# Optimization experiments

Hardware: AMD Instinct MI355X
Metric: run time of the kernel (lower is better)

The kernel has to match this reference:

```python
import jax, jax.numpy as jnp
import numpy as np

B, C, H, W = 8, 512, 48, 48
DK = C // 8            # query/key dim
L = max(H, W)          # rel_pos_length == H == W
R = 2 * L - 1          # num relative shifts
N = H * W
EPS = 1e-5


def setup_inputs() -> dict:
    key = jax.random.key(0)
    ks = jax.random.split(key, 20)
    d = {
        "x": jax.random.normal(ks[0], (B, C, H, W), jnp.float32),
        "Wq": jax.random.normal(ks[1], (DK, C), jnp.float32) * 0.02,
        "bq": jnp.zeros((DK,), jnp.float32),
        "q_scale": jnp.ones((DK,), jnp.float32),
        "q_bias": jnp.zeros((DK,), jnp.float32),
        "Wk": jax.random.normal(ks[2], (DK, C), jnp.float32) * 0.02,
        "bk": jnp.zeros((DK,), jnp.float32),
        "k_scale": jnp.ones((DK,), jnp.float32),
        "k_bias": jnp.zeros((DK,), jnp.float32),
        "Wv": jax.random.normal(ks[3], (C, C), jnp.float32) * 0.02,
        "bv": jnp.zeros((C,), jnp.float32),
        "v_scale": jnp.ones((C,), jnp.float32),
        "v_bias": jnp.zeros((C,), jnp.float32),
        "rel_rows": jax.random.normal(ks[4], (R, DK), jnp.float32),
        "rel_columns": jax.random.normal(ks[5], (R, DK), jnp.float32),
        "bnr_scale": jnp.ones((C,), jnp.float32),
        "bnr_bias": jnp.zeros((C,), jnp.float32),
        "bnc_scale": jnp.ones((C,), jnp.float32),
        "bnc_bias": jnp.zeros((C,), jnp.float32),
        # gamma is a learned scalar (init 0 in torch; nonzero here so output != x)
        "gamma": jax.random.normal(ks[6], (1,), jnp.float32) * 0.1,
    }
    return d


def _bn(y, scale, bias):
    # train-mode BatchNorm2d: batch stats over (B,H,W), biased variance
    m = jnp.mean(y, axis=(0, 2, 3))
    v = jnp.mean((y - m[None, :, None, None]) ** 2, axis=(0, 2, 3))
    yn = (y - m[None, :, None, None]) * jax.lax.rsqrt(v + EPS)[None, :, None, None]
    return yn * scale[None, :, None, None] + bias[None, :, None, None]


def _conv_bn_relu(x, Wc, bc, scale, bias):
    y = jnp.einsum('bchw,oc->bohw', x, Wc) + bc[None, :, None, None]  # 1x1 conv
    return jax.nn.relu(_bn(y, scale, bias))


def _rel_P(l, rel_table):
    # compute_reindexing_tensor reduces to a one-hot over shift (i - x) since
    # |i-x| <= L always holds when L == l; Ih @ rel_table == gather by shift.
    x = jnp.arange(l)[:, None]
    i = jnp.arange(l)[None, :]
    idx = i - x + (L - 1)                 # (l, l) in [0, 2L-2]
    return rel_table[idx]                 # (l, l, DK)


def reference(x, Wq, bq, q_scale, q_bias, Wk, bk, k_scale, k_bias,
              Wv, bv, v_scale, v_bias, rel_rows, rel_columns,
              bnr_scale, bnr_bias, bnc_scale, bnc_bias, gamma):
    q = _conv_bn_relu(x, Wq, bq, q_scale, q_bias).reshape(B, DK, N)   # proj_query^T
    k = _conv_bn_relu(x, Wk, bk, k_scale, k_bias).reshape(B, DK, N)
    v = _conv_bn_relu(x, Wv, bv, v_scale, v_bias).reshape(B, C, N)

    energy = jnp.einsum('bdn,bdm->bnm', q, k)        # (B,N,N) = Q^T K (unscaled)
    attention = jax.nn.softmax(energy, axis=-1)
    out = jnp.einsum('bcj,bij->bci', v, attention)   # V A^T
    attn_mask = out.reshape(B, C, H, W)

    # relative position terms: Eh = V (Ph Q^T), Ew = V (Pw Q^T)
    Ph = _rel_P(H, rel_rows).reshape(N, DK)          # (N,DK) since H==W
    Mh = jnp.einsum('nd,bdm->bnm', Ph, q)
    Eh = jnp.einsum('bcn,bnm->bcm', v, Mh).reshape(B, C, H, W)
    Eh = _bn(Eh, bnr_scale, bnr_bias)

    Pw = _rel_P(W, rel_columns).reshape(N, DK)
    Mw = jnp.einsum('nd,bdm->bnm', Pw, q)
    Ew = jnp.einsum('bcn,bnm->bcm', v, Mw).reshape(B, C, H, W)
    Ew = _bn(Ew, bnc_scale, bnc_bias)

    attn_mask = attn_mask + Eh + Ew
    return gamma[0] * attn_mask + x
```

## Files before the change

### kernel.cpp

```cpp
#include <hip/hip_runtime.h>
#include <math.h>

#define BB   8
#define CIN  512
#define NSP  2304
#define OCH  640
#define LL   48

typedef __attribute__((ext_vector_type(8))) short bf16x8;
typedef __attribute__((ext_vector_type(8))) unsigned short u16x8;
typedef __attribute__((ext_vector_type(4))) float f32x4;

__device__ inline unsigned short f2bf(float f) {
  unsigned int u = __float_as_uint(f);
  unsigned int r = (u + 0x7fffu + ((u >> 16) & 1u)) >> 16;
  return (unsigned short)r;
}
__device__ inline float bf2f(unsigned short h) {
  return __uint_as_float(((unsigned int)h) << 16);
}


#define STAGE128x64(GP, LD, LDSN)                                              \
  {                                                                            \
    const unsigned short* gsrc_ = (GP);                                        \
    _Pragma("unroll") for (int cc_ = 0; cc_ < 4; cc_++) {                      \
      int base_ = w * 2048 + cc_ * 512;                                        \
      int row_ = w * 32 + cc_ * 8 + rsub;                                      \
      __builtin_amdgcn_global_load_lds(                                        \
          (const __attribute__((address_space(1))) void*)(gsrc_ +              \
              (size_t)row_ * (LD) + scolb),                                    \
          (__attribute__((address_space(3))) void*)&(LDSN)[base_], 16, 0, 0);  \
    }                                                                          \
  }

#define STAGE8(GPA, LDA, LA, GPB, LDB, LB)                                     \
  {                                                                            \
    if (w < 4) {                                                               \
      const unsigned short* gsrc_ = (GPA);                                     \
      _Pragma("unroll") for (int cc_ = 0; cc_ < 4; cc_++) {                    \
        int base_ = w * 2048 + cc_ * 512;                                      \
        int row_ = w * 32 + cc_ * 8 + rsub;                                    \
        __builtin_amdgcn_global_load_lds(                                      \
            (const __attribute__((address_space(1))) void*)(gsrc_ +            \
                (size_t)row_ * (LDA) + scolb),                                 \
            (__attribute__((address_space(3))) void*)&(LA)[base_], 16, 0, 0);  \
      }                                                                        \
    } else {                                                                   \
      const unsigned short* gsrc_ = (GPB);                                     \
      int w2_ = w - 4;                                                         \
      _Pragma("unroll") for (int cc_ = 0; cc_ < 4; cc_++) {                    \
        int base_ = w2_ * 2048 + cc_ * 512;                                    \
        int row_ = w2_ * 32 + cc_ * 8 + rsub;                                  \
        __builtin_amdgcn_global_load_lds(                                      \
            (const __attribute__((address_space(1))) void*)(gsrc_ +            \
                (size_t)row_ * (LDB) + scolb),                                 \
            (__attribute__((address_space(3))) void*)&(LB)[base_], 16, 0, 0);  \
      }                                                                        \
    }                                                                          \
  }

#define MFMA_STEP(APTR, BPTR)                                                  \
  _Pragma("unroll") for (int kk_ = 0; kk_ < 2; kk_++) {                        \
    bf16x8 af_[4], bf_[4];                                                     \
    int kcol_ = (((kk_ * 4 + (lane >> 4)) ^ (lane & 7)) * 8);                  \
    _Pragma("unroll") for (int m_ = 0; m_ < 4; m_++)                           \
      af_[m_] = *(const bf16x8*)&(APTR)[(wr * 64 + m_ * 16 + (lane & 15)) * 64 + kcol_]; \
    _Pragma("unroll") for (int n_ = 0; n_ < 4; n_++)                           \
      bf_[n_] = *(const bf16x8*)&(BPTR)[(wc * 64 + n_ * 16 + (lane & 15)) * 64 + kcol_]; \
    _Pragma("unroll") for (int m_ = 0; m_ < 4; m_++)                           \
      _Pragma("unroll") for (int n_ = 0; n_ < 4; n_++)                         \
        acc[m_][n_] = __builtin_amdgcn_mfma_f32_16x16x32_bf16(                 \
            af_[m_], bf_[n_], acc[m_][n_], 0, 0, 0);                           \
  }

#define MFMA_STEP8(APTR, BPTR)                                                 \
  _Pragma("unroll") for (int kk_ = 0; kk_ < 2; kk_++) {                        \
    bf16x8 af_[4], bf_[2];                                                     \
    int kcol_ = (((kk_ * 4 + (lane >> 4)) ^ (lane & 7)) * 8);                  \
    _Pragma("unroll") for (int m_ = 0; m_ < 4; m_++)                           \
      af_[m_] = *(const bf16x8*)&(APTR)[(wr * 64 + m_ * 16 + (lane & 15)) * 64 + kcol_]; \
    _Pragma("unroll") for (int n_ = 0; n_ < 2; n_++)                           \
      bf_[n_] = *(const bf16x8*)&(BPTR)[(wc * 32 + n_ * 16 + (lane & 15)) * 64 + kcol_]; \
    _Pragma("unroll") for (int m_ = 0; m_ < 4; m_++)                           \
      _Pragma("unroll") for (int n_ = 0; n_ < 2; n_++)                         \
        acc[m_][n_] = __builtin_amdgcn_mfma_f32_16x16x32_bf16(                 \
            af_[m_], bf_[n_], acc[m_][n_], 0, 0, 0);                           \
  }

#define MFMA_PROLOG()                                                          \
  const int tid = threadIdx.x;                                                 \
  const int lane = tid & 63;                                                   \
  const int w = tid >> 6;                                                      \
  const int wr = w >> 1, wc = w & 1;                                           \
  const int rsub = lane >> 3;                                                  \
  const int scolb = ((lane & 7) ^ rsub) * 8;                                   \
  f32x4 acc[4][4] = {};                                                        \
  (void)scolb; (void)rsub; (void)wr; (void)wc;

__global__ __launch_bounds__(256) void prep_all(
    const float* __restrict__ Wq, const float* __restrict__ bq,
    const float* __restrict__ Wk, const float* __restrict__ bk,
    const float* __restrict__ Wv, const float* __restrict__ bv,
    const float* __restrict__ rel_rows, const float* __restrict__ rel_cols,
    unsigned short* __restrict__ Wstb, float* __restrict__ bst,
    unsigned short* __restrict__ Pcatb) {
  int idx = blockIdx.x * 256 + threadIdx.x;
  if (idx < OCH * CIN) {
    int row = idx >> 9;
    float val;
    if (row < 64)       val = Wq[idx];
    else if (row < 128) val = Wk[idx - (64 << 9)];
    else                val = Wv[idx - (128 << 9)];
    Wstb[idx] = f2bf(val);
    if (idx < OCH) {
      float bval;
      if (idx < 64)       bval = bq[idx];
      else if (idx < 128) bval = bk[idx - 64];
      else                bval = bv[idx - 128];
      bst[idx] = bval;
    }
  } else {
    int p = idx - OCH * CIN;
    int dd = p / NSP;
    int n = p - dd * NSP;
    int xr = n / LL;
    int ic = n - xr * LL;
    int shift = ic - xr + (LL - 1);
    float val = (dd < 64) ? rel_rows[shift * 64 + dd]
                          : rel_cols[shift * 64 + (dd - 64)];
    Pcatb[p] = f2bf(val);
  }
}

__global__ __launch_bounds__(256) void transpose_x(
    const float* __restrict__ x, unsigned short* __restrict__ xTb) {
  __shared__ float t[64][65];
  const int n0 = blockIdx.x * 64;
  const int c0 = blockIdx.y * 64;
  const int b = blockIdx.z;
  const int j = threadIdx.x & 63;
  const int g = threadIdx.x >> 6;
  const float* xp = x + (size_t)b * CIN * NSP;
#pragma unroll
  for (int i = 0; i < 16; i++) {
    int cl = g * 16 + i;
    t[cl][j] = xp[(size_t)(c0 + cl) * NSP + n0 + j];
  }
  __syncthreads();
  unsigned short* op = xTb + (size_t)b * NSP * CIN;
#pragma unroll
  for (int i = 0; i < 16; i++) {
    int nl = g * 16 + i;
    op[(size_t)(n0 + nl) * CIN + c0 + j] = f2bf(t[j][nl]);
  }
}

__global__ __launch_bounds__(256) void proj_mfma(
    const unsigned short* __restrict__ Wstb, const float* __restrict__ bst,
    const unsigned short* __restrict__ xTb, unsigned short* __restrict__ y16,
    float* __restrict__ part1, float* __restrict__ part2) {
  __shared__ unsigned short As[2][8192];
  __shared__ unsigned short Bs[2][8192];
  int sw = ((blockIdx.x & 7) * 90) + (blockIdx.x >> 3);
  const int rb = sw % 5;
  const int nb = (sw / 5) % 18;
  const int b = sw / 90;
  const int r0 = rb * 128;
  const int n0 = nb * 128;
  MFMA_PROLOG();
  const unsigned short* A = Wstb + (size_t)r0 * CIN;
  const unsigned short* B = xTb + (size_t)b * NSP * CIN + (size_t)n0 * CIN;

  STAGE128x64(A, CIN, As[0]);
  STAGE128x64(B, CIN, Bs[0]);
  STAGE128x64(A + 64, CIN, As[1]);
  STAGE128x64(B + 64, CIN, Bs[1]);
  asm volatile("s_waitcnt vmcnt(8)" ::: "memory");
  __builtin_amdgcn_sched_barrier(0);
  __builtin_amdgcn_s_barrier();

  int cur = 0;
  for (int t = 0; t < 8; ++t) {
    __builtin_amdgcn_s_setprio(1);
    MFMA_STEP(As[cur], Bs[cur]);
    __builtin_amdgcn_s_setprio(0);
    __builtin_amdgcn_sched_barrier(0);
    __builtin_amdgcn_s_barrier();
    if (t + 2 < 8) {
      STAGE128x64(A + (t + 2) * 64, CIN, As[cur]);
      STAGE128x64(B + (t + 2) * 64, CIN, Bs[cur]);
      asm volatile("s_waitcnt vmcnt(8)" ::: "memory");
    } else {
      asm volatile("s_waitcnt vmcnt(0)" ::: "memory");
    }
    __builtin_amdgcn_sched_barrier(0);
    __builtin_amdgcn_s_barrier();
    cur ^= 1;
  }

  float* sp = (float*)&As[0][0];
#pragma unroll
  for (int m = 0; m < 4; m++) {
#pragma unroll
    for (int r = 0; r < 4; r++) {
      int rl = wr * 64 + m * 16 + (lane >> 4) * 4 + r;
      int row = r0 + rl;
      float bias = bst[row];
      float s1 = 0.f, s2 = 0.f;
#pragma unroll
      for (int n = 0; n < 4; n++) {
        float yv = acc[m][n][r] + bias;
        s1 += yv;
        s2 += yv * yv;
        y16[((size_t)b * OCH + row) * NSP + n0 + wc * 64 + n * 16 + (lane & 15)] = f2bf(yv);
      }
#pragma unroll
      for (int off = 1; off < 16; off <<= 1) {
        s1 += __shfl_xor(s1, off);
        s2 += __shfl_xor(s2, off);
      }
      if ((lane & 15) == 0) {
        sp[rl * 2 + wc] = s1;
        sp[256 + rl * 2 + wc] = s2;
      }
    }
  }
  __syncthreads();
  if (tid < 128) {
    size_t pbase = ((size_t)b * 18 + nb) * OCH + r0 + tid;
    part1[pbase] = sp[tid * 2] + sp[tid * 2 + 1];
    part2[pbase] = sp[256 + tid * 2] + sp[256 + tid * 2 + 1];
  }
}

__global__ __launch_bounds__(256) void bn_finalize(
    const float* __restrict__ part1, const float* __restrict__ part2,
    const float* __restrict__ qs_, const float* __restrict__ qb_,
    const float* __restrict__ ks_, const float* __restrict__ kb_,
    const float* __restrict__ vs_, const float* __restrict__ vb_,
    float* __restrict__ chanA, float* __restrict__ chanB) {
  const int ch = blockIdx.x;
  const int tid = threadIdx.x;
  float s1 = 0.f, s2 = 0.f;
  for (int t = tid; t < 144; t += 256) {
    s1 += part1[(size_t)t * OCH + ch];
    s2 += part2[(size_t)t * OCH + ch];
  }
  __shared__ float sb[8];
#pragma unroll
  for (int off = 32; off > 0; off >>= 1) {
    s1 += __shfl_down(s1, off);
    s2 += __shfl_down(s2, off);
  }
  int lane = tid & 63, wid = tid >> 6;
  if (lane == 0) { sb[wid] = s1; sb[4 + wid] = s2; }
  __syncthreads();
  if (tid == 0) {
    float ts  = sb[0] + sb[1] + sb[2] + sb[3];
    float ts2 = sb[4] + sb[5] + sb[6] + sb[7];
    const float inv = 1.f / (float)(BB * NSP);
    float mean = ts * inv;
    float var  = ts2 * inv - mean * mean;
    float scale, bias;
    if (ch < 64)       { scale = qs_[ch];       bias = qb_[ch]; }
    else if (ch < 128) { scale = ks_[ch - 64];  bias = kb_[ch - 64]; }
    else               { scale = vs_[ch - 128]; bias = vb_[ch - 128]; }
    float a = scale * rsqrtf(var + 1e-5f);
    chanA[ch] = a;
    chanB[ch] = bias - mean * a;
  }
}

__global__ __launch_bounds__(256) void bnrelu_all(
    unsigned short* __restrict__ y16, const float* __restrict__ chanA,
    const float* __restrict__ chanB) {
  size_t i = ((size_t)blockIdx.x * 256 + threadIdx.x) * 8;
  int ch = (int)((i / NSP) % OCH);
  float a = chanA[ch], bo = chanB[ch];
  ushort4 u0 = *(ushort4*)&y16[i];
  ushort4 u1 = *(ushort4*)&y16[i + 4];
  ushort4 o0, o1;
  o0.x = f2bf(fmaxf(0.f, a * bf2f(u0.x) + bo));
  o0.y = f2bf(fmaxf(0.f, a * bf2f(u0.y) + bo));
  o0.z = f2bf(fmaxf(0.f, a * bf2f(u0.z) + bo));
  o0.w = f2bf(fmaxf(0.f, a * bf2f(u0.w) + bo));
  o1.x = f2bf(fmaxf(0.f, a * bf2f(u1.x) + bo));
  o1.y = f2bf(fmaxf(0.f, a * bf2f(u1.y) + bo));
  o1.z = f2bf(fmaxf(0.f, a * bf2f(u1.z) + bo));
  o1.w = f2bf(fmaxf(0.f, a * bf2f(u1.w) + bo));
  *(ushort4*)&y16[i] = o0;
  *(ushort4*)&y16[i + 4] = o1;
}

__global__ __launch_bounds__(256) void tr_qk(
    const unsigned short* __restrict__ y16, unsigned short* __restrict__ qTb,
    unsigned short* __restrict__ kTb) {
  __shared__ unsigned short t[64][72];
  const int n0 = blockIdx.x * 64;
  const int qk = blockIdx.y;
  const int b = blockIdx.z;
  const int j = threadIdx.x & 63;
  const int g = threadIdx.x >> 6;
#pragma unroll
  for (int i = 0; i < 16; i++) {
    int cl = g * 16 + i;
    t[cl][j] = y16[((size_t)b * OCH + qk * 64 + cl) * NSP + n0 + j];
  }
  __syncthreads();
  unsigned short* out = (qk == 0) ? qTb : kTb;
#pragma unroll
  for (int i = 0; i < 16; i++) {
    int nl = g * 16 + i;
    out[((size_t)b * NSP + n0 + nl) * 64 + j] = t[j][nl];
  }
}

__global__ __launch_bounds__(256) void qsum_kernel(
    const unsigned short* __restrict__ y16, float* __restrict__ qs) {
  int bd = blockIdx.x;
  int b = bd >> 6, d = bd & 63;
  const ushort4* p = (const ushort4*)(y16 + ((size_t)b * OCH + d) * NSP);
  float s = 0.f;
  for (int t = threadIdx.x; t < NSP / 4; t += 256) {
    ushort4 u = p[t];
    s += bf2f(u.x) + bf2f(u.y) + bf2f(u.z) + bf2f(u.w);
  }
  __shared__ float sb[4];
#pragma unroll
  for (int off = 32; off > 0; off >>= 1) s += __shfl_down(s, off);
  int lane = threadIdx.x & 63, wid = threadIdx.x >> 6;
  if (lane == 0) sb[wid] = s;
  __syncthreads();
  if (threadIdx.x == 0) qs[bd] = sb[0] + sb[1] + sb[2] + sb[3];
}

__global__ __launch_bounds__(256) void gq_mfma(
    const unsigned short* __restrict__ y16, float* __restrict__ Gqp) {
  __shared__ float wlds[4 * 4096];
  const int bx = blockIdx.x;
  const int b = bx >> 2, kc = bx & 3;
  const int tid = threadIdx.x;
  const int lane = tid & 63;
  const int w = tid >> 6;
  const unsigned short* q = y16 + (size_t)b * OCH * NSP;
  f32x4 acc[4][4] = {};
  for (int k0 = kc * 576 + w * 32; k0 < (kc + 1) * 576; k0 += 128) {
    bf16x8 fr[4];
#pragma unroll
    for (int f = 0; f < 4; f++) {
      int row = f * 16 + (lane & 15);
      fr[f] = *(const bf16x8*)&q[(size_t)row * NSP + k0 + (lane >> 4) * 8];
    }
#pragma unroll
    for (int fm = 0; fm < 4; fm++)
#pragma unroll
      for (int fn = 0; fn < 4; fn++)
        acc[fm][fn] = __builtin_amdgcn_mfma_f32_16x16x32_bf16(
            fr[fm], fr[fn], acc[fm][fn], 0, 0, 0);
  }
#pragma unroll
  for (int fm = 0; fm < 4; fm++)
#pragma unroll
    for (int fn = 0; fn < 4; fn++)
#pragma unroll
      for (int r = 0; r < 4; r++) {
        int d = fm * 16 + (lane >> 4) * 4 + r;
        int e = fn * 16 + (lane & 15);
        wlds[w * 4096 + d * 64 + e] = acc[fm][fn][r];
      }
  __syncthreads();
  for (int t = tid; t < 4096; t += 256)
    Gqp[(size_t)bx * 4096 + t] =
        wlds[t] + wlds[4096 + t] + wlds[8192 + t] + wlds[12288 + t];
}

__global__ __launch_bounds__(256) void energy_mfma(
    const unsigned short* __restrict__ qTb, const unsigned short* __restrict__ kTb,
    unsigned short* __restrict__ Pp, float* __restrict__ Ppart) {
  __shared__ unsigned short As[8192];
  __shared__ unsigned short Bs[8192];
  int sw = ((blockIdx.x & 7) * 324) + (blockIdx.x >> 3);
  const int jb = sw % 18;
  const int ib = (sw / 18) % 18;
  const int b = sw / 324;
  const int i0 = ib * 128;
  const int j0 = jb * 128;
  MFMA_PROLOG();
  STAGE128x64(qTb + ((size_t)b * NSP + i0) * 64, 64, As);
  STAGE128x64(kTb + ((size_t)b * NSP + j0) * 64, 64, Bs);
  __syncthreads();
  MFMA_STEP(As, Bs);
  __syncthreads();
  float* sp = (float*)As;
  unsigned short* pp = Pp + (size_t)b * NSP * NSP;
#pragma unroll
  for (int m = 0; m < 4; m++) {
#pragma unroll
    for (int r = 0; r < 4; r++) {
      int rl = wr * 64 + m * 16 + (lane >> 4) * 4 + r;
      int i = i0 + rl;
      float s1 = 0.f;
#pragma unroll
      for (int n = 0; n < 4; n++) {
        int j = j0 + wc * 64 + n * 16 + (lane & 15);
        unsigned short h = f2bf(__expf(acc[m][n][r]));
        pp[(size_t)i * NSP + j] = h;
        s1 += bf2f(h);
      }
#pragma unroll
      for (int off = 1; off < 16; off <<= 1) s1 += __shfl_xor(s1, off);
      if ((lane & 15) == 0) sp[rl * 2 + wc] = s1;
    }
  }
  __syncthreads();
  if (tid < 128)
    Ppart[((size_t)b * 18 + jb) * NSP + i0 + tid] = sp[tid * 2] + sp[tid * 2 + 1];
}

__global__ __launch_bounds__(256) void zred_kernel(
    const float* __restrict__ Ppart, float* __restrict__ rZ) {
  int row = blockIdx.x * 256 + threadIdx.x;
  int b = row / NSP, i = row % NSP;
  float s = 0.f;
#pragma unroll
  for (int jb = 0; jb < 18; jb++) s += Ppart[((size_t)b * 18 + jb) * NSP + i];
  rZ[row] = 1.f / s;
}

__global__ __launch_bounds__(256) void up_mfma(
    const unsigned short* __restrict__ y16, const unsigned short* __restrict__ Pcatb,
    float* __restrict__ Upart) {
  __shared__ unsigned short As[2][8192];
  __shared__ unsigned short Bs[2][8192];
  int sw = ((blockIdx.x & 7) * 24) + (blockIdx.x >> 3);
  const int cb = sw % 4;
  const int kc = (sw / 4) % 6;
  const int b = sw / 24;
  const int c0 = cb * 128;
  MFMA_PROLOG();
  const unsigned short* A = y16 + ((size_t)b * OCH + 128 + c0) * NSP + kc * 384;
  const unsigned short* B = Pcatb + kc * 384;

  STAGE128x64(A, NSP, As[0]);
  STAGE128x64(B, NSP, Bs[0]);
  STAGE128x64(A + 64, NSP, As[1]);
  STAGE128x64(B + 64, NSP, Bs[1]);
  asm volatile("s_waitcnt vmcnt(8)" ::: "memory");
  __builtin_amdgcn_sched_barrier(0);
  __builtin_amdgcn_s_barrier();

  int cur = 0;
  for (int t = 0; t < 6; ++t) {
    __builtin_amdgcn_s_setprio(1);
    MFMA_STEP(As[cur], Bs[cur]);
    __builtin_amdgcn_s_setprio(0);
    __builtin_amdgcn_sched_barrier(0);
    __builtin_amdgcn_s_barrier();
    if (t + 2 < 6) {
      STAGE128x64(A + (t + 2) * 64, NSP, As[cur]);
      STAGE128x64(B + (t + 2) * 64, NSP, Bs[cur]);
      asm volatile("s_waitcnt vmcnt(8)" ::: "memory");
    } else {
      asm volatile("s_waitcnt vmcnt(0)" ::: "memory");
    }
    __builtin_amdgcn_sched_barrier(0);
    __builtin_amdgcn_s_barrier();
    cur ^= 1;
  }

  float* up = Upart + ((size_t)kc * BB + b) * CIN * 128 + (size_t)c0 * 128;
#pragma unroll
  for (int m = 0; m < 4; m++)
#pragma unroll
    for (int r = 0; r < 4; r++) {
      int rl = wr * 64 + m * 16 + (lane >> 4) * 4 + r;
#pragma unroll
      for (int n = 0; n < 4; n++) {
        int col = wc * 64 + n * 16 + (lane & 15);
        up[(size_t)rl * 128 + col] = acc[m][n][r];
      }
    }
}

__global__ __launch_bounds__(256) void rel_finalize(
    const float* __restrict__ Upart, const float* __restrict__ Gqp,
    const float* __restrict__ qs,
    const float* __restrict__ bnr_s, const float* __restrict__ bnr_b,
    const float* __restrict__ bnc_s, const float* __restrict__ bnc_b,
    float* __restrict__ offc, unsigned short* __restrict__ Ucb) {
  const int c = blockIdx.x;
  const int tid = threadIdx.x;
  __shared__ float U[8][128];
  __shared__ float ghw[2];
  for (int t = tid; t < 1024; t += 256) {
    int b = t >> 7, dd = t & 127;
    float s = 0.f;
#pragma unroll
    for (int kc = 0; kc < 6; kc++)
      s += Upart[(((size_t)kc * BB + b) * CIN + c) * 128 + dd];
    U[b][dd] = s;
  }
  __syncthreads();
  if (tid < 64) {
    const int d = tid;
    float s1h = 0.f, s2h = 0.f, s1w = 0.f, s2w = 0.f;
    for (int b = 0; b < BB; b++) {
      float uh = U[b][d], uw = U[b][64 + d];
      float th = 0.f, tw = 0.f;
#pragma unroll
      for (int kc = 0; kc < 4; kc++) {
        const float* G = Gqp + ((size_t)(b * 4 + kc)) * 4096 + d * 64;
        for (int e = 0; e < 64; e++) {
          float g = G[e];
          th += g * U[b][e];
          tw += g * U[b][64 + e];
        }
      }
      float qsd = qs[b * 64 + d];
      s1h += uh * qsd;
      s2h += uh * th;
      s1w += uw * qsd;
      s2w += uw * tw;
    }
#pragma unroll
    for (int off = 32; off > 0; off >>= 1) {
      s1h += __shfl_down(s1h, off);
      s2h += __shfl_down(s2h, off);
      s1w += __shfl_down(s1w, off);
      s2w += __shfl_down(s2w, off);
    }
    if (d == 0) {
      const float inv = 1.f / (float)(BB * NSP);
      float mh = s1h * inv, vh = s2h * inv - mh * mh;
      float mw = s1w * inv, vw = s2w * inv - mw * mw;
      float gch = bnr_s[c] * rsqrtf(vh + 1e-5f);
      float gcw = bnc_s[c] * rsqrtf(vw + 1e-5f);
      ghw[0] = gch;
      ghw[1] = gcw;
      offc[c] = (bnr_b[c] - mh * gch) + (bnc_b[c] - mw * gcw);
    }
  }
  __syncthreads();
  for (int t = tid; t < 512; t += 256) {
    int b = t >> 6, d = t & 63;
    Ucb[((size_t)b * CIN + c) * 64 + d] =
        f2bf(U[b][d] * ghw[0] + U[b][64 + d] * ghw[1]);
  }
}

__global__ __launch_bounds__(512) void attn_fused_gemm(
    const unsigned short* __restrict__ y16,
    const unsigned short* __restrict__ Pp,
    const float* __restrict__ rZ,
    const unsigned short* __restrict__ Ucb,
    const unsigned short* __restrict__ qTb,
    const float* __restrict__ offc,
    const float* __restrict__ gammap,
    const float* __restrict__ x,
    float* __restrict__ dst) {
  __shared__ unsigned short As[2][8192];
  __shared__ unsigned short Bs[2][8192];
  int sw = ((blockIdx.x & 7) * 72) + (blockIdx.x >> 3);
  const int cb = sw % 4;
  const int ib = (sw / 4) % 18;
  const int b = sw / 72;
  const int c0 = cb * 128;
  const int i0 = ib * 128;
  const int tid = threadIdx.x;
  const int lane = tid & 63;
  const int w = tid >> 6;
  const int wr = w >> 2, wc = w & 3;
  const int rsub = lane >> 3;
  const int scolb = ((lane & 7) ^ rsub) * 8;
  f32x4 acc[4][2] = {};

  const unsigned short* A = y16 + ((size_t)b * OCH + 128 + c0) * NSP;
  const unsigned short* B = Pp + (size_t)b * NSP * NSP + (size_t)i0 * NSP;
  const unsigned short* A2 = Ucb + (size_t)b * CIN * 64 + (size_t)c0 * 64;
  const unsigned short* B2 = qTb + (size_t)b * NSP * 64 + (size_t)i0 * 64;

  STAGE8(A, NSP, As[0], B, NSP, Bs[0]);
  STAGE8(A + 64, NSP, As[1], B + 64, NSP, Bs[1]);
  asm volatile("s_waitcnt vmcnt(4)" ::: "memory");
  __builtin_amdgcn_sched_barrier(0);
  __builtin_amdgcn_s_barrier();

  int cur = 0;
  for (int tt = 0; tt < 37; ++tt) {
    if (tt == 36) {
#pragma unroll
      for (int n = 0; n < 2; n++) {
        float rz = rZ[(size_t)b * NSP + i0 + wc * 32 + n * 16 + (lane & 15)];
#pragma unroll
        for (int m = 0; m < 4; m++)
#pragma unroll
          for (int r = 0; r < 4; r++) acc[m][n][r] *= rz;
      }
    }
    __builtin_amdgcn_s_setprio(1);
    MFMA_STEP8(As[cur], Bs[cur]);
    __builtin_amdgcn_s_setprio(0);
    __builtin_amdgcn_sched_barrier(0);
    __builtin_amdgcn_s_barrier();
    if (tt + 2 < 36) {
      STAGE8(A + (tt + 2) * 64, NSP, As[cur], B + (tt + 2) * 64, NSP, Bs[cur]);
      asm volatile("s_waitcnt vmcnt(4)" ::: "memory");
    } else if (tt + 2 == 36) {
      STAGE8(A2, 64, As[cur], B2, 64, Bs[cur]);
      asm volatile("s_waitcnt vmcnt(4)" ::: "memory");
    } else {
      asm volatile("s_waitcnt vmcnt(0)" ::: "memory");
    }
    __builtin_amdgcn_sched_barrier(0);
    __builtin_amdgcn_s_barrier();
    cur ^= 1;
  }

  const float gmm = gammap[0];
  const float* xp = x + (size_t)b * CIN * NSP;
  float* dp = dst + (size_t)b * CIN * NSP;
#pragma unroll
  for (int m = 0; m < 4; m++) {
#pragma unroll
    for (int r = 0; r < 4; r++) {
      int c = c0 + wr * 64 + m * 16 + (lane >> 4) * 4 + r;
      float off = offc[c];
#pragma unroll
      for (int n = 0; n < 2; n++) {
        int i = i0 + wc * 32 + n * 16 + (lane & 15);
        size_t o = (size_t)c * NSP + i;
        dp[o] = gmm * (acc[m][n][r] + off) + xp[o];
      }
    }
  }
}

extern "C" void kernel_launch(void* const* d_in, const int* in_sizes, int n_in,
                              void* d_out, int out_size, void* d_ws, size_t ws_size,
                              hipStream_t stream) {
  const float* x        = (const float*)d_in[0];
  const float* Wq       = (const float*)d_in[1];
  const float* bq       = (const float*)d_in[2];
  const float* q_scale  = (const float*)d_in[3];
  const float* q_bias   = (const float*)d_in[4];
  const float* Wk       = (const float*)d_in[5];
  const float* bk       = (const float*)d_in[6];
  const float* k_scale  = (const float*)d_in[7];
  const float* k_bias   = (const float*)d_in[8];
  const float* Wv       = (const float*)d_in[9];
  const float* bv       = (const float*)d_in[10];
  const float* v_scale  = (const float*)d_in[11];
  const float* v_bias   = (const float*)d_in[12];
  const float* rel_rows = (const float*)d_in[13];
  const float* rel_cols = (const float*)d_in[14];
  const float* bnr_s    = (const float*)d_in[15];
  const float* bnr_b    = (const float*)d_in[16];
  const float* bnc_s    = (const float*)d_in[17];
  const float* bnc_b    = (const float*)d_in[18];
  const float* gamma    = (const float*)d_in[19];
  float* dst = (float*)d_out;

  float* ws = (float*)d_ws;
  size_t o = 0;
  unsigned short* Wstb = (unsigned short*)(ws + o); o += (size_t)OCH * CIN / 2;
  float* bst    = ws + o; o += 1024;
  float* chanA  = ws + o; o += 1024;
  float* chanB  = ws + o; o += 1024;
  unsigned short* Pcatb = (unsigned short*)(ws + o); o += (size_t)128 * NSP / 2;
  unsigned short* y16 = (unsigned short*)(ws + o); o += (size_t)BB * OCH * NSP / 2;
  unsigned short* xTb = (unsigned short*)(ws + o); o += (size_t)BB * NSP * CIN / 2;
  unsigned short* Pp  = (unsigned short*)(ws + o); o += (size_t)BB * NSP * NSP / 2;
  float* Ppart  = ws + o; o += (size_t)BB * 18 * NSP;
  float* rZ     = ws + o; o += (size_t)BB * NSP;
  float* Upart  = ws + o; o += (size_t)6 * BB * CIN * 128;
  float* Gqp    = ws + o; o += (size_t)32 * 4096;
  float* part1  = ws + o; o += (size_t)BB * 18 * OCH;
  float* part2  = ws + o; o += (size_t)BB * 18 * OCH;
  float* qs     = ws + o; o += 1024;
  float* offc   = ws + o; o += 1024;
  unsigned short* qTb = (unsigned short*)(ws + o); o += (size_t)BB * NSP * 64 / 2;
  unsigned short* kTb = (unsigned short*)(ws + o); o += (size_t)BB * NSP * 64 / 2;
  unsigned short* Ucb = (unsigned short*)(ws + o); o += (size_t)BB * CIN * 64 / 2;

  prep_all<<<(OCH * CIN + 128 * NSP) / 256, 256, 0, stream>>>(
      Wq, bq, Wk, bk, Wv, bv, rel_rows, rel_cols, Wstb, bst, Pcatb);
  transpose_x<<<dim3(NSP / 64, CIN / 64, BB), 256, 0, stream>>>(x, xTb);

  proj_mfma<<<720, 256, 0, stream>>>(Wstb, bst, xTb, y16, part1, part2);
  bn_finalize<<<OCH, 256, 0, stream>>>(part1, part2, q_scale, q_bias, k_scale,
                                       k_bias, v_scale, v_bias, chanA, chanB);
  bnrelu_all<<<(int)((size_t)BB * OCH * NSP / 8 / 256), 256, 0, stream>>>(y16, chanA, chanB);
  tr_qk<<<dim3(NSP / 64, 2, BB), 256, 0, stream>>>(y16, qTb, kTb);
  qsum_kernel<<<BB * 64, 256, 0, stream>>>(y16, qs);
  gq_mfma<<<32, 256, 0, stream>>>(y16, Gqp);

  energy_mfma<<<2592, 256, 0, stream>>>(qTb, kTb, Pp, Ppart);
  zred_kernel<<<BB * NSP / 256, 256, 0, stream>>>(Ppart, rZ);

  up_mfma<<<192, 256, 0, stream>>>(y16, Pcatb, Upart);
  rel_finalize<<<CIN, 256, 0, stream>>>(Upart, Gqp, qs, bnr_s, bnr_b,
                                        bnc_s, bnc_b, offc, Ucb);

  attn_fused_gemm<<<576, 512, 0, stream>>>(y16, Pp, rZ, Ucb, qTb, offc, gamma, x, dst);
}
```

Measured before the change: 237.9 us.

## Fuse BN-ReLU with Q/K transpose, fold Z reduction into final GEMM, restructure prefetch

Merges the BN+ReLU pass and the Q/K transpose into one kernel that keeps the Q/K tile in shared memory, which removes a full re-read of y16 for the transpose. The softmax normalizer reduction moves into the prologue of the final attention GEMM, so the separate zred kernel and the rZ buffer go away. The GEMM loops also change from a two-stage-ahead prefetch issued after the barrier to a one-stage-ahead prefetch issued before the MFMAs, with a full vmcnt(0) wait each step. That pipeline change may expose more load latency, and each of the 576 final blocks now recomputes its 128 reciprocals.

```diff
diff --git a/kernel.cpp b/kernel.cpp
--- a/kernel.cpp
+++ b/kernel.cpp
@@ -174,26 +174,20 @@
 
   STAGE128x64(A, CIN, As[0]);
   STAGE128x64(B, CIN, Bs[0]);
-  STAGE128x64(A + 64, CIN, As[1]);
-  STAGE128x64(B + 64, CIN, Bs[1]);
-  asm volatile("s_waitcnt vmcnt(8)" ::: "memory");
+  asm volatile("s_waitcnt vmcnt(0)" ::: "memory");
   __builtin_amdgcn_sched_barrier(0);
   __builtin_amdgcn_s_barrier();
 
   int cur = 0;
   for (int t = 0; t < 8; ++t) {
+    if (t + 1 < 8) {
+      STAGE128x64(A + (t + 1) * 64, CIN, As[cur ^ 1]);
+      STAGE128x64(B + (t + 1) * 64, CIN, Bs[cur ^ 1]);
+    }
     __builtin_amdgcn_s_setprio(1);
     MFMA_STEP(As[cur], Bs[cur]);
     __builtin_amdgcn_s_setprio(0);
-    __builtin_amdgcn_sched_barrier(0);
-    __builtin_amdgcn_s_barrier();
-    if (t + 2 < 8) {
-      STAGE128x64(A + (t + 2) * 64, CIN, As[cur]);
-      STAGE128x64(B + (t + 2) * 64, CIN, Bs[cur]);
-      asm volatile("s_waitcnt vmcnt(8)" ::: "memory");
-    } else {
-      asm volatile("s_waitcnt vmcnt(0)" ::: "memory");
-    }
+    asm volatile("s_waitcnt vmcnt(0)" ::: "memory");
     __builtin_amdgcn_sched_barrier(0);
     __builtin_amdgcn_s_barrier();
     cur ^= 1;
@@ -272,47 +266,51 @@
   }
 }
 
-__global__ __launch_bounds__(256) void bnrelu_all(
+__global__ __launch_bounds__(256) void bn_post(
     unsigned short* __restrict__ y16, const float* __restrict__ chanA,
-    const float* __restrict__ chanB) {
-  size_t i = ((size_t)blockIdx.x * 256 + threadIdx.x) * 8;
-  int ch = (int)((i / NSP) % OCH);
-  float a = chanA[ch], bo = chanB[ch];
-  ushort4 u0 = *(ushort4*)&y16[i];
-  ushort4 u1 = *(ushort4*)&y16[i + 4];
-  ushort4 o0, o1;
-  o0.x = f2bf(fmaxf(0.f, a * bf2f(u0.x) + bo));
-  o0.y = f2bf(fmaxf(0.f, a * bf2f(u0.y) + bo));
-  o0.z = f2bf(fmaxf(0.f, a * bf2f(u0.z) + bo));
-  o0.w = f2bf(fmaxf(0.f, a * bf2f(u0.w) + bo));
-  o1.x = f2bf(fmaxf(0.f, a * bf2f(u1.x) + bo));
-  o1.y = f2bf(fmaxf(0.f, a * bf2f(u1.y) + bo));
-  o1.z = f2bf(fmaxf(0.f, a * bf2f(u1.z) + bo));
-  o1.w = f2bf(fmaxf(0.f, a * bf2f(u1.w) + bo));
-  *(ushort4*)&y16[i] = o0;
-  *(ushort4*)&y16[i + 4] = o1;
-}
-
-__global__ __launch_bounds__(256) void tr_qk(
-    const unsigned short* __restrict__ y16, unsigned short* __restrict__ qTb,
+    const float* __restrict__ chanB, unsigned short* __restrict__ qTb,
     unsigned short* __restrict__ kTb) {
-  __shared__ unsigned short t[64][72];
+  __shared__ unsigned short qk[128][64];
   const int n0 = blockIdx.x * 64;
-  const int qk = blockIdx.y;
-  const int b = blockIdx.z;
-  const int j = threadIdx.x & 63;
-  const int g = threadIdx.x >> 6;
-#pragma unroll
-  for (int i = 0; i < 16; i++) {
-    int cl = g * 16 + i;
-    t[cl][j] = y16[((size_t)b * OCH + qk * 64 + cl) * NSP + n0 + j];
-  }
-  __syncthreads();
-  unsigned short* out = (qk == 0) ? qTb : kTb;
-#pragma unroll
-  for (int i = 0; i < 16; i++) {
-    int nl = g * 16 + i;
-    out[((size_t)b * NSP + n0 + nl) * 64 + j] = t[j][nl];
+  const int b = blockIdx.y;
+  const int tid = threadIdx.x;
+#pragma unroll
+  for (int k = 0; k < 20; k++) {
+    int v = tid + k * 256;
+    int ch = v >> 3;
+    int n8 = (v & 7) * 8;
+    size_t off = ((size_t)b * OCH + ch) * NSP + n0 + n8;
+    float a = chanA[ch], bo = chanB[ch];
+    ushort4 u0 = *(ushort4*)&y16[off];
+    ushort4 u1 = *(ushort4*)&y16[off + 4];
+    ushort4 o0, o1;
+    o0.x = f2bf(fmaxf(0.f, a * bf2f(u0.x) + bo));
+    o0.y = f2bf(fmaxf(0.f, a * bf2f(u0.y) + bo));
+    o0.z = f2bf(fmaxf(0.f, a * bf2f(u0.z) + bo));
+    o0.w = f2bf(fmaxf(0.f, a * bf2f(u0.w) + bo));
+    o1.x = f2bf(fmaxf(0.f, a * bf2f(u1.x) + bo));
+    o1.y = f2bf(fmaxf(0.f, a * bf2f(u1.y) + bo));
+    o1.z = f2bf(fmaxf(0.f, a * bf2f(u1.z) + bo));
+    o1.w = f2bf(fmaxf(0.f, a * bf2f(u1.w) + bo));
+    *(ushort4*)&y16[off] = o0;
+    *(ushort4*)&y16[off + 4] = o1;
+    if (ch < 128) {
+      *(ushort4*)&qk[ch][n8] = o0;
+      *(ushort4*)&qk[ch][n8 + 4] = o1;
+    }
+  }
+  __syncthreads();
+#pragma unroll
+  for (int it = 0; it < 4; it++) {
+    int combo = (tid >> 6) + it * 4;
+    int plane = combo >> 3;
+    int dg = combo & 7;
+    int nl = tid & 63;
+    unsigned short tmp[8];
+#pragma unroll
+    for (int d = 0; d < 8; d++) tmp[d] = qk[plane * 64 + dg * 8 + d][nl];
+    unsigned short* out = (plane == 0) ? qTb : kTb;
+    *(u16x8*)&out[((size_t)b * NSP + n0 + nl) * 64 + dg * 8] = *(u16x8*)tmp;
   }
 }
 
@@ -418,16 +416,6 @@
     Ppart[((size_t)b * 18 + jb) * NSP + i0 + tid] = sp[tid * 2] + sp[tid * 2 + 1];
 }
 
-__global__ __launch_bounds__(256) void zred_kernel(
-    const float* __restrict__ Ppart, float* __restrict__ rZ) {
-  int row = blockIdx.x * 256 + threadIdx.x;
-  int b = row / NSP, i = row % NSP;
-  float s = 0.f;
-#pragma unroll
-  for (int jb = 0; jb < 18; jb++) s += Ppart[((size_t)b * 18 + jb) * NSP + i];
-  rZ[row] = 1.f / s;
-}
-
 __global__ __launch_bounds__(256) void up_mfma(
     const unsigned short* __restrict__ y16, const unsigned short* __restrict__ Pcatb,
     float* __restrict__ Upart) {
@@ -444,26 +432,20 @@
 
   STAGE128x64(A, NSP, As[0]);
   STAGE128x64(B, NSP, Bs[0]);
-  STAGE128x64(A + 64, NSP, As[1]);
-  STAGE128x64(B + 64, NSP, Bs[1]);
-  asm volatile("s_waitcnt vmcnt(8)" ::: "memory");
+  asm volatile("s_waitcnt vmcnt(0)" ::: "memory");
   __builtin_amdgcn_sched_barrier(0);
   __builtin_amdgcn_s_barrier();
 
   int cur = 0;
   for (int t = 0; t < 6; ++t) {
+    if (t + 1 < 6) {
+      STAGE128x64(A + (t + 1) * 64, NSP, As[cur ^ 1]);
+      STAGE128x64(B + (t + 1) * 64, NSP, Bs[cur ^ 1]);
+    }
     __builtin_amdgcn_s_setprio(1);
     MFMA_STEP(As[cur], Bs[cur]);
     __builtin_amdgcn_s_setprio(0);
-    __builtin_amdgcn_sched_barrier(0);
-    __builtin_amdgcn_s_barrier();
-    if (t + 2 < 6) {
-      STAGE128x64(A + (t + 2) * 64, NSP, As[cur]);
-      STAGE128x64(B + (t + 2) * 64, NSP, Bs[cur]);
-      asm volatile("s_waitcnt vmcnt(8)" ::: "memory");
-    } else {
-      asm volatile("s_waitcnt vmcnt(0)" ::: "memory");
-    }
+    asm volatile("s_waitcnt vmcnt(0)" ::: "memory");
     __builtin_amdgcn_sched_barrier(0);
     __builtin_amdgcn_s_barrier();
     cur ^= 1;
@@ -552,7 +534,7 @@
 __global__ __launch_bounds__(512) void attn_fused_gemm(
     const unsigned short* __restrict__ y16,
     const unsigned short* __restrict__ Pp,
-    const float* __restrict__ rZ,
+    const float* __restrict__ Ppart,
     const unsigned short* __restrict__ Ucb,
     const unsigned short* __restrict__ qTb,
     const float* __restrict__ offc,
@@ -561,6 +543,7 @@
     float* __restrict__ dst) {
   __shared__ unsigned short As[2][8192];
   __shared__ unsigned short Bs[2][8192];
+  __shared__ float rzl[128];
   int sw = ((blockIdx.x & 7) * 72) + (blockIdx.x >> 3);
   const int cb = sw % 4;
   const int ib = (sw / 4) % 18;
@@ -581,17 +564,28 @@
   const unsigned short* B2 = qTb + (size_t)b * NSP * 64 + (size_t)i0 * 64;
 
   STAGE8(A, NSP, As[0], B, NSP, Bs[0]);
-  STAGE8(A + 64, NSP, As[1], B + 64, NSP, Bs[1]);
-  asm volatile("s_waitcnt vmcnt(4)" ::: "memory");
+  if (tid < 128) {
+    float s = 0.f;
+#pragma unroll
+    for (int jb = 0; jb < 18; jb++)
+      s += Ppart[((size_t)b * 18 + jb) * NSP + i0 + tid];
+    rzl[tid] = 1.f / s;
+  }
+  asm volatile("s_waitcnt vmcnt(0)" ::: "memory");
   __builtin_amdgcn_sched_barrier(0);
   __builtin_amdgcn_s_barrier();
 
   int cur = 0;
   for (int tt = 0; tt < 37; ++tt) {
+    if (tt + 1 < 36) {
+      STAGE8(A + (tt + 1) * 64, NSP, As[cur ^ 1], B + (tt + 1) * 64, NSP, Bs[cur ^ 1]);
+    } else if (tt + 1 == 36) {
+      STAGE8(A2, 64, As[cur ^ 1], B2, 64, Bs[cur ^ 1]);
+    }
     if (tt == 36) {
 #pragma unroll
       for (int n = 0; n < 2; n++) {
-        float rz = rZ[(size_t)b * NSP + i0 + wc * 32 + n * 16 + (lane & 15)];
+        float rz = rzl[wc * 32 + n * 16 + (lane & 15)];
 #pragma unroll
         for (int m = 0; m < 4; m++)
 #pragma unroll
@@ -601,17 +595,7 @@
     __builtin_amdgcn_s_setprio(1);
     MFMA_STEP8(As[cur], Bs[cur]);
     __builtin_amdgcn_s_setprio(0);
-    __builtin_amdgcn_sched_barrier(0);
-    __builtin_amdgcn_s_barrier();
-    if (tt + 2 < 36) {
-      STAGE8(A + (tt + 2) * 64, NSP, As[cur], B + (tt + 2) * 64, NSP, Bs[cur]);
-      asm volatile("s_waitcnt vmcnt(4)" ::: "memory");
-    } else if (tt + 2 == 36) {
-      STAGE8(A2, 64, As[cur], B2, 64, Bs[cur]);
-      asm volatile("s_waitcnt vmcnt(4)" ::: "memory");
-    } else {
-      asm volatile("s_waitcnt vmcnt(0)" ::: "memory");
-    }
+    asm volatile("s_waitcnt vmcnt(0)" ::: "memory");
     __builtin_amdgcn_sched_barrier(0);
     __builtin_amdgcn_s_barrier();
     cur ^= 1;
@@ -672,7 +656,6 @@
   unsigned short* xTb = (unsigned short*)(ws + o); o += (size_t)BB * NSP * CIN / 2;
   unsigned short* Pp  = (unsigned short*)(ws + o); o += (size_t)BB * NSP * NSP / 2;
   float* Ppart  = ws + o; o += (size_t)BB * 18 * NSP;
-  float* rZ     = ws + o; o += (size_t)BB * NSP;
   float* Upart  = ws + o; o += (size_t)6 * BB * CIN * 128;
   float* Gqp    = ws + o; o += (size_t)32 * 4096;
   float* part1  = ws + o; o += (size_t)BB * 18 * OCH;
@@ -690,17 +673,15 @@
   proj_mfma<<<720, 256, 0, stream>>>(Wstb, bst, xTb, y16, part1, part2);
   bn_finalize<<<OCH, 256, 0, stream>>>(part1, part2, q_scale, q_bias, k_scale,
                                        k_bias, v_scale, v_bias, chanA, chanB);
-  bnrelu_all<<<(int)((size_t)BB * OCH * NSP / 8 / 256), 256, 0, stream>>>(y16, chanA, chanB);
-  tr_qk<<<dim3(NSP / 64, 2, BB), 256, 0, stream>>>(y16, qTb, kTb);
+  bn_post<<<dim3(36, BB), 256, 0, stream>>>(y16, chanA, chanB, qTb, kTb);
   qsum_kernel<<<BB * 64, 256, 0, stream>>>(y16, qs);
   gq_mfma<<<32, 256, 0, stream>>>(y16, Gqp);
 
   energy_mfma<<<2592, 256, 0, stream>>>(qTb, kTb, Pp, Ppart);
-  zred_kernel<<<BB * NSP / 256, 256, 0, stream>>>(Ppart, rZ);
 
   up_mfma<<<192, 256, 0, stream>>>(y16, Pcatb, Upart);
   rel_finalize<<<CIN, 256, 0, stream>>>(Upart, Gqp, qs, bnr_s, bnr_b,
                                         bnc_s, bnc_b, offc, Ucb);
 
-  attn_fused_gemm<<<576, 512, 0, stream>>>(y16, Pp, rZ, Ucb, qTb, offc, gamma, x, dst);
-}
+  attn_fused_gemm<<<576, 512, 0, stream>>>(y16, Pp, Ppart, Ucb, qTb, offc, gamma, x, dst);
+}
```

Measured after the change: 240.2 us. No clear change (+1.0%).
